# Kernel tuning notes

Hardware: AMD Instinct MI355X
Metric: run time of the kernel (lower is better)

The kernel has to match this reference:

```python
import jax, jax.numpy as jnp
import numpy as np

EPS = 1e-08


def _norm(H, add):
    # Faithful to GTN.norm: transpose, mask/set diagonal, row-normalize by degree, transpose back.
    # The original O(N^3) mm(deg_inv_diag, H) is expressed as an O(N^2) row scaling (same math).
    Ht = H.T
    n = Ht.shape[0]
    eye = jnp.eye(n, dtype=H.dtype)
    Ht = Ht * (1.0 - eye)
    if add:
        Ht = Ht + eye
    deg = jnp.sum(Ht, axis=1)
    deg_inv = jnp.where(deg == 0, 0.0, 1.0 / (deg + EPS))
    return (deg_inv[:, None] * Ht).T


def _gtconv(A, w):
    # A: [E, N, N]; w: [C, E, 1, 1] -> softmax over E, weighted sum of adjacency channels.
    s = jax.nn.softmax(w[:, :, 0, 0], axis=1)  # [C, E]
    return jnp.einsum('ce,eij->cij', s, A)     # [C, N, N]


def setup_inputs() -> dict:
    key = jax.random.key(0)
    k = jax.random.split(key, 6)
    E, N, C, w_in, w_out = 5, 2048, 2, 256, 64
    A = jax.random.uniform(k[0], (E, N, N), dtype=jnp.float32)
    X = jax.random.normal(k[1], (N, w_in), dtype=jnp.float32)
    conv_w_l0_1 = jax.random.normal(k[2], (C, E, 1, 1), dtype=jnp.float32)
    conv_w_l0_2 = jax.random.normal(k[3], (C, E, 1, 1), dtype=jnp.float32)
    conv_w_l1 = jax.random.normal(k[4], (C, E, 1, 1), dtype=jnp.float32)
    gcn_weight = jax.random.normal(k[5], (w_in, w_out), dtype=jnp.float32) * (1.0 / np.sqrt(w_in))
    return {"A": A, "X": X, "conv_w_l0_1": conv_w_l0_1, "conv_w_l0_2": conv_w_l0_2,
            "conv_w_l1": conv_w_l1, "gcn_weight": gcn_weight}


def reference(A, X, conv_w_l0_1, conv_w_l0_2, conv_w_l1, gcn_weight):
    N = A.shape[1]
    # Layer 0 (first=True): two GTConvs, meta-path composition via bmm.
    a = _gtconv(A, conv_w_l0_1)            # [C, N, N]
    b = _gtconv(A, conv_w_l0_2)            # [C, N, N]
    H = jnp.einsum('cij,cjk->cik', a, b)   # [C, N, N]
    # Layer 1 (first=False): normalize per channel, then compose with new conv.
    H = jax.vmap(lambda h: _norm(h, False))(H)
    a1 = _gtconv(A, conv_w_l1)
    H = jnp.einsum('cij,cjk->cik', H, a1)
    # GCN readout per channel: mm(norm_add(H_c).T, X @ W), relu, concat along features.
    Xw = X @ gcn_weight                     # [N, w_out]
    Hn = jax.vmap(lambda h: _norm(h, True))(H)   # [C, N, N]
    Xc = jax.nn.relu(jnp.einsum('cji,jk->cik', Hn, Xw))  # [C, N, w_out]
    X_ = jnp.transpose(Xc, (1, 0, 2)).reshape(N, -1)     # [N, C*w_out]
    return X_
```

## Files before the change

kernel.cpp:

```cpp
#include <hip/hip_runtime.h>
#include <cstdint>
#include <cstddef>

typedef unsigned short u16;
typedef __attribute__((ext_vector_type(8))) short short8;
typedef __attribute__((ext_vector_type(4))) float v4f;

static constexpr size_t NN = (size_t)2048 * 2048;
#define N2 2048

typedef __attribute__((address_space(1))) const unsigned int guint;
typedef __attribute__((address_space(3))) unsigned int luint;

__device__ __forceinline__ float b2f_bits(uint32_t hi) { union { uint32_t u; float f; } v; v.u = hi; return v.f; }
__device__ __forceinline__ float b2f(u16 x) { return b2f_bits((uint32_t)x << 16); }
__device__ __forceinline__ u16 f2b(float f) {
  union { float f; uint32_t u; } v; v.f = f;
  uint32_t r = v.u + 0x7fffu + ((v.u >> 16) & 1u);
  return (u16)(r >> 16);
}
__device__ __forceinline__ uint2 pack4(const float* f) {
  uint2 u;
  u.x = (uint32_t)f2b(f[0]) | ((uint32_t)f2b(f[1]) << 16);
  u.y = (uint32_t)f2b(f[2]) | ((uint32_t)f2b(f[3]) << 16);
  return u;
}
__device__ __forceinline__ uint4 pack8(const float* f) {
  uint4 u;
  u.x = (uint32_t)f2b(f[0]) | ((uint32_t)f2b(f[1]) << 16);
  u.y = (uint32_t)f2b(f[2]) | ((uint32_t)f2b(f[3]) << 16);
  u.z = (uint32_t)f2b(f[4]) | ((uint32_t)f2b(f[5]) << 16);
  u.w = (uint32_t)f2b(f[6]) | ((uint32_t)f2b(f[7]) << 16);
  return u;
}

__global__ __launch_bounds__(256, 6) void conv_kernel(
    const float* __restrict__ A, const float* __restrict__ w1,
    const float* __restrict__ w2, const float* __restrict__ w3,
    const float* __restrict__ X, const float* __restrict__ W,
    u16* __restrict__ abf, u16* __restrict__ bbt, u16* __restrict__ a1t,
    u16* __restrict__ Xwt)
{
  __shared__ float lb[32][33];
  __shared__ float la[32][33];
  const int t = threadIdx.x;
  const int i0 = blockIdx.y * 32, j0 = blockIdx.x * 32;

  float s1[2][5], s2[2][5], s3[2][5];
  {
    const float* wsrc[3] = { w1, w2, w3 };
    float (*sdst[3])[5] = { s1, s2, s3 };
    for (int q = 0; q < 3; ++q)
      for (int c = 0; c < 2; ++c) {
        float v[5], m = -1e30f, sum = 0.f;
        for (int e = 0; e < 5; ++e) { v[e] = wsrc[q][c * 5 + e]; m = fmaxf(m, v[e]); }
        for (int e = 0; e < 5; ++e) { v[e] = expf(v[e] - m); sum += v[e]; }
        for (int e = 0; e < 5; ++e) sdst[q][c][e] = v[e] / sum;
      }
  }

  const int row = t >> 3;
  const int c4 = (t & 7) * 4;
  float cst[2][4];

  {
    float fa[5][4];
    for (int e = 0; e < 5; ++e) {
      float4 v = *(const float4*)(A + (size_t)e * NN + (size_t)(i0 + row) * N2 + (j0 + c4));
      fa[e][0] = v.x; fa[e][1] = v.y; fa[e][2] = v.z; fa[e][3] = v.w;
    }
    for (int c = 0; c < 2; ++c) {
      float av[4] = {0,0,0,0}, bv[4] = {0,0,0,0}, cv[4] = {0,0,0,0};
      for (int e = 0; e < 5; ++e)
        #pragma unroll
        for (int u = 0; u < 4; ++u) {
          av[u] += s1[c][e] * fa[e][u];
          bv[u] += s2[c][e] * fa[e][u];
          cv[u] += s3[c][e] * fa[e][u];
        }
      *(uint2*)(abf + (size_t)c * NN + (size_t)(i0 + row) * N2 + (j0 + c4)) = pack4(av);
      float* ldst = (c == 0) ? &lb[row][c4] : &la[row][c4];
      #pragma unroll
      for (int u = 0; u < 4; ++u) ldst[u] = bv[u];
      #pragma unroll
      for (int u = 0; u < 4; ++u) cst[c][u] = cv[u];
    }
  }
  __syncthreads();
  {
    float t0[4], t1[4];
    #pragma unroll
    for (int u = 0; u < 4; ++u) { t0[u] = lb[c4 + u][row]; t1[u] = la[c4 + u][row]; }
    *(uint2*)(bbt + 0 * NN + (size_t)(j0 + row) * N2 + (i0 + c4)) = pack4(t0);
    *(uint2*)(bbt + 1 * NN + (size_t)(j0 + row) * N2 + (i0 + c4)) = pack4(t1);
  }
  __syncthreads();
  #pragma unroll
  for (int u = 0; u < 4; ++u) { lb[row][c4 + u] = cst[0][u]; la[row][c4 + u] = cst[1][u]; }
  __syncthreads();
  {
    float t0[4], t1[4];
    #pragma unroll
    for (int u = 0; u < 4; ++u) { t0[u] = lb[c4 + u][row]; t1[u] = la[c4 + u][row]; }
    *(uint2*)(a1t + 0 * NN + (size_t)(j0 + row) * N2 + (i0 + c4)) = pack4(t0);
    *(uint2*)(a1t + 1 * NN + (size_t)(j0 + row) * N2 + (i0 + c4)) = pack4(t1);
  }
  if (blockIdx.y < 8) {
    const int n = (int)(blockIdx.y * 64 + blockIdx.x) * 4 + (t >> 6);
    const int k = t & 63;
    float acc = 0.f;
    for (int m = 0; m < 256; ++m)
      acc += X[n * 256 + m] * W[m * 64 + k];
    Xwt[(size_t)k * N2 + n] = f2b(acc);
  }
}

template<bool TOUT>
__global__ __launch_bounds__(256, 5) void gemm_kernel(
    const u16* __restrict__ Ain, const u16* __restrict__ Btin,
    u16* __restrict__ Cout, float* __restrict__ csp, float* __restrict__ diag)
{
  const int c = blockIdx.z;
  const u16* Ac = Ain + (size_t)c * NN;
  const u16* Bc = Btin + (size_t)c * NN;
  const int m0 = blockIdx.y * 128, n0 = blockIdx.x * 64;
  const int t = threadIdx.x, w = t >> 6, lane = t & 63;
  const int quad = lane >> 4, r = lane & 15;
  __shared__ u16 SM[128 * 64 + 64 * 64];
  u16* As = SM;
  u16* Bs = SM + 128 * 64;

  v4f zero4 = { 0.f, 0.f, 0.f, 0.f };
  v4f acc[2][4];
  #pragma unroll
  for (int i = 0; i < 2; ++i)
    #pragma unroll
    for (int j = 0; j < 4; ++j) acc[i][j] = zero4;

  const int srow = lane >> 3;
  const int sgran = (lane & 7) ^ srow;

  for (int kt = 0; kt < 2048; kt += 64) {
    __syncthreads();
    #pragma unroll
    for (int i = 0; i < 4; ++i) {
      const int chunk = i * 4 + w;
      const u16* ga = Ac + (size_t)(m0 + chunk * 8 + srow) * N2 + kt + sgran * 8;
      __builtin_amdgcn_global_load_lds((guint*)ga, (luint*)(As + chunk * 512), 16, 0, 0);
    }
    #pragma unroll
    for (int i = 0; i < 2; ++i) {
      const int chunk = i * 4 + w;
      const u16* gb = Bc + (size_t)(n0 + chunk * 8 + srow) * N2 + kt + sgran * 8;
      __builtin_amdgcn_global_load_lds((guint*)gb, (luint*)(Bs + chunk * 512), 16, 0, 0);
    }
    __syncthreads();
    #pragma unroll
    for (int ks = 0; ks < 2; ++ks) {
      const int sl = ((ks * 4 + quad) ^ (r & 7)) * 8;
      short8 af[2], bf[4];
      #pragma unroll
      for (int i = 0; i < 2; ++i)
        af[i] = *(const short8*)(As + (w * 32 + i * 16 + r) * 64 + sl);
      #pragma unroll
      for (int j = 0; j < 4; ++j)
        bf[j] = *(const short8*)(Bs + (j * 16 + r) * 64 + sl);
      #pragma unroll
      for (int i = 0; i < 2; ++i)
        #pragma unroll
        for (int j = 0; j < 4; ++j)
          acc[i][j] = __builtin_amdgcn_mfma_f32_16x16x32_bf16(af[i], bf[j], acc[i][j], 0, 0, 0);
    }
  }
  if ((int)(blockIdx.x >> 1) == (int)blockIdx.y) {
    #pragma unroll
    for (int i = 0; i < 2; ++i) {
      const int rowg = m0 + w * 32 + i * 16 + quad * 4;
      #pragma unroll
      for (int j = 0; j < 4; ++j) {
        const int colg = n0 + j * 16 + r;
        #pragma unroll
        for (int g = 0; g < 4; ++g)
          if (rowg + g == colg) diag[c * N2 + colg] = acc[i][j][g];
      }
    }
  }
  if constexpr (!TOUT) {
    u16* Cc = Cout + (size_t)c * NN;
    #pragma unroll
    for (int i = 0; i < 2; ++i) {
      const int rowg = m0 + w * 32 + i * 16 + quad * 4;
      #pragma unroll
      for (int j = 0; j < 4; ++j) {
        const int colg = n0 + j * 16 + r;
        #pragma unroll
        for (int g = 0; g < 4; ++g)
          Cc[(size_t)(rowg + g) * N2 + colg] = f2b(acc[i][j][g]);
      }
    }
  }
  float s[4];
  #pragma unroll
  for (int j = 0; j < 4; ++j) {
    s[j] = 0.f;
    #pragma unroll
    for (int i = 0; i < 2; ++i)
      #pragma unroll
      for (int g = 0; g < 4; ++g) s[j] += acc[i][j][g];
    s[j] += __shfl_xor(s[j], 16);
    s[j] += __shfl_xor(s[j], 32);
  }
  __syncthreads();
  float* csl = (float*)SM;
  if (quad == 0) {
    #pragma unroll
    for (int j = 0; j < 4; ++j) csl[w * 64 + j * 16 + r] = s[j];
  }
  __syncthreads();
  if (t < 64) {
    const float v = csl[t] + csl[64 + t] + csl[128 + t] + csl[192 + t];
    csp[((size_t)(c * 16) + blockIdx.y) * N2 + n0 + t] = v;
  }
  if constexpr (TOUT) {
    __syncthreads();
    u16* tb = SM;
    #pragma unroll
    for (int i = 0; i < 2; ++i) {
      #pragma unroll
      for (int j = 0; j < 4; ++j) {
        #pragma unroll
        for (int g = 0; g < 4; ++g)
          tb[(j * 16 + r) * 136 + (w * 32 + i * 16 + quad * 4 + g)] = f2b(acc[i][j][g]);
      }
    }
    __syncthreads();
    u16* Cc = Cout + (size_t)c * NN;
    const int rown = t >> 2, seg = t & 3;
    const u16* ps = tb + rown * 136 + seg * 32;
    uint4* pd = (uint4*)(Cc + (size_t)(n0 + rown) * N2 + m0 + seg * 32);
    pd[0] = ((const uint4*)ps)[0];
    pd[1] = ((const uint4*)ps)[1];
    pd[2] = ((const uint4*)ps)[2];
    pd[3] = ((const uint4*)ps)[3];
  }
}

__global__ void colinv_kernel(const float* __restrict__ csp, const float* __restrict__ diag, float* __restrict__ ci)
{
  const int idx = blockIdx.x * 256 + threadIdx.x;
  float cs = 0.f;
  const int c = idx >> 11, q = idx & 2047;
  #pragma unroll
  for (int s = 0; s < 16; ++s) cs += csp[((size_t)(c * 16) + s) * N2 + q];
  const float deg = cs - diag[idx];
  ci[idx] = (deg == 0.f) ? 0.f : 1.f / (deg + 1e-8f);
}

__global__ __launch_bounds__(256) void scale_kernel(const u16* __restrict__ H, const float* __restrict__ ci, u16* __restrict__ Hn)
{
  const int idx = blockIdx.x * 256 + threadIdx.x;
  const int q0 = (idx & 255) * 8;
  const int p = (idx >> 8) & 2047;
  const int c = idx >> 19;
  const u16* src = H + (size_t)c * NN + (size_t)p * N2 + q0;
  const float* cv = ci + c * N2 + q0;
  uint4 hu = *(const uint4*)src;
  float h[8];
  h[0] = b2f_bits(hu.x << 16); h[1] = b2f_bits(hu.x & 0xffff0000u);
  h[2] = b2f_bits(hu.y << 16); h[3] = b2f_bits(hu.y & 0xffff0000u);
  h[4] = b2f_bits(hu.z << 16); h[5] = b2f_bits(hu.z & 0xffff0000u);
  h[6] = b2f_bits(hu.w << 16); h[7] = b2f_bits(hu.w & 0xffff0000u);
  float f[8];
  #pragma unroll
  for (int u = 0; u < 8; ++u) {
    float v = h[u] * cv[u];
    f[u] = (q0 + u == p) ? 0.f : v;
  }
  *(uint4*)(Hn + (size_t)c * NN + (size_t)p * N2 + q0) = pack8(f);
}

__global__ __launch_bounds__(256) void tgemm_kernel(
    const u16* __restrict__ H2t, const u16* __restrict__ Xwt, float* __restrict__ Tp)
{
  const int c = blockIdx.z, split = blockIdx.y;
  const int m0 = blockIdx.x * 128;
  const u16* Ac = H2t + (size_t)c * NN;
  const int t = threadIdx.x, w = t >> 6, lane = t & 63;
  const int quad = lane >> 4, r = lane & 15;
  __shared__ u16 As[128 * 64];
  __shared__ u16 Bs[64 * 64];

  v4f zero4 = { 0.f, 0.f, 0.f, 0.f };
  v4f acc[2][4];
  #pragma unroll
  for (int i = 0; i < 2; ++i)
    #pragma unroll
    for (int j = 0; j < 4; ++j) acc[i][j] = zero4;

  const int srow = lane >> 3;
  const int sgran = (lane & 7) ^ srow;

  for (int kk = 0; kk < 2; ++kk) {
    const int kt = split * 128 + kk * 64;
    __syncthreads();
    #pragma unroll
    for (int i = 0; i < 4; ++i) {
      const int chunk = i * 4 + w;
      const u16* ga = Ac + (size_t)(m0 + chunk * 8 + srow) * N2 + kt + sgran * 8;
      __builtin_amdgcn_global_load_lds((guint*)ga, (luint*)(As + chunk * 512), 16, 0, 0);
    }
    #pragma unroll
    for (int i = 0; i < 2; ++i) {
      const int chunk = i * 4 + w;
      const u16* gb = Xwt + (size_t)(chunk * 8 + srow) * N2 + kt + sgran * 8;
      __builtin_amdgcn_global_load_lds((guint*)gb, (luint*)(Bs + chunk * 512), 16, 0, 0);
    }
    __syncthreads();
    #pragma unroll
    for (int ks = 0; ks < 2; ++ks) {
      const int sl = ((ks * 4 + quad) ^ (r & 7)) * 8;
      short8 af[2], bf[4];
      #pragma unroll
      for (int i = 0; i < 2; ++i)
        af[i] = *(const short8*)(As + (w * 32 + i * 16 + r) * 64 + sl);
      #pragma unroll
      for (int j = 0; j < 4; ++j)
        bf[j] = *(const short8*)(Bs + (j * 16 + r) * 64 + sl);
      #pragma unroll
      for (int i = 0; i < 2; ++i)
        #pragma unroll
        for (int j = 0; j < 4; ++j)
          acc[i][j] = __builtin_amdgcn_mfma_f32_16x16x32_bf16(af[i], bf[j], acc[i][j], 0, 0, 0);
    }
  }
  const size_t pbase = (size_t)(split * 2 + c) * 2048;
  #pragma unroll
  for (int i = 0; i < 2; ++i) {
    const int rowg = m0 + w * 32 + i * 16 + quad * 4;
    #pragma unroll
    for (int j = 0; j < 4; ++j) {
      const int colg = j * 16 + r;
      #pragma unroll
      for (int g = 0; g < 4; ++g)
        Tp[(pbase + rowg + g) * 64 + colg] = acc[i][j][g];
    }
  }
}

__global__ void epilogue_kernel(const float* __restrict__ Tp, const float* __restrict__ cspb,
                                const float* __restrict__ diag2, const u16* __restrict__ Xwt,
                                float* __restrict__ out)
{
  const int idx = blockIdx.x * 256 + threadIdx.x;
  const int k = idx & 63;
  const int c = (idx >> 6) & 1;
  const int i = idx >> 7;
  float T = 0.f, cs = 0.f;
  #pragma unroll
  for (int s = 0; s < 16; ++s) {
    T  += Tp[((size_t)(s * 2 + c) * 2048 + i) * 64 + k];
    cs += cspb[((size_t)(c * 16) + s) * N2 + i];
  }
  const float hd = diag2[c * N2 + i];
  const float xw = b2f(Xwt[(size_t)k * N2 + i]);
  const float deg = cs - hd + 1.0f;
  const float dinv = (deg == 0.f) ? 0.f : 1.f / (deg + 1e-8f);
  float v = dinv * (T - hd * xw + xw);
  v = v > 0.f ? v : 0.f;
  out[(size_t)i * 128 + c * 64 + k] = v;
}

extern "C" void kernel_launch(void* const* d_in, const int* in_sizes, int n_in,
                              void* d_out, int out_size, void* d_ws, size_t ws_size,
                              hipStream_t stream) {
  const float* A  = (const float*)d_in[0];
  const float* X  = (const float*)d_in[1];
  const float* w1 = (const float*)d_in[2];
  const float* w2 = (const float*)d_in[3];
  const float* w3 = (const float*)d_in[4];
  const float* W  = (const float*)d_in[5];
  float* out = (float*)d_out;
  char* ws = (char*)d_ws;

  u16*   abf   = (u16*)(ws + 0);
  u16*   bbt   = (u16*)(ws + 16777216);
  u16*   a1t   = (u16*)(ws + 33554432);
  u16*   Hbf   = (u16*)(ws + 50331648);
  u16*   Hn    = (u16*)(ws + 67108864);
  u16*   Xwt   = (u16*)(ws + 83886080);
  float* cspa  = (float*)(ws + 84148224);
  float* cspb  = (float*)(ws + 84410368);
  float* diag1 = (float*)(ws + 84672512);
  float* diag2 = (float*)(ws + 84688896);
  float* ci1   = (float*)(ws + 84705280);
  u16*   H2t   = (u16*)(ws + 0);
  float* Tp    = (float*)(ws + 16777216);

  conv_kernel<<<dim3(64, 64), 256, 0, stream>>>(A, w1, w2, w3, X, W, abf, bbt, a1t, Xwt);
  gemm_kernel<false><<<dim3(32, 16, 2), 256, 0, stream>>>(abf, bbt, Hbf, cspa, diag1);
  colinv_kernel<<<16, 256, 0, stream>>>(cspa, diag1, ci1);
  scale_kernel<<<4096, 256, 0, stream>>>(Hbf, ci1, Hn);
  gemm_kernel<true><<<dim3(32, 16, 2), 256, 0, stream>>>(Hn, a1t, H2t, cspb, diag2);
  tgemm_kernel<<<dim3(16, 16, 2), 256, 0, stream>>>(H2t, Xwt, Tp);
  epilogue_kernel<<<1024, 256, 0, stream>>>(Tp, cspb, diag2, Xwt, out);
}
```

Measured before the change: 266.5 us.

## Split-K the two large GEMMs into two partial outputs merged downstream

Each big N×N GEMM now runs as a split-K over two halves of K, doubling the grid from 1024 to 2048 blocks for better CU occupancy. Each half writes its own bf16 partial product, column-sum partials and diagonal. Consumers (colinv, scale, tgemm, epilogue) sum the two partials, and launch bounds rise to 6 waves per SIMD. The cost is extra memory traffic for writing and re-reading the doubled partial matrices, plus a bf16 rounding of each partial before the add. The workspace layout is reshuffled with several dead pointer assignments.

Result: slower. 353.7 us (+32.7%).

```diff
diff --git a/kernel.cpp b/kernel.cpp
--- a/kernel.cpp
+++ b/kernel.cpp
@@ -32,6 +32,19 @@
   u.z = (uint32_t)f2b(f[4]) | ((uint32_t)f2b(f[5]) << 16);
   u.w = (uint32_t)f2b(f[6]) | ((uint32_t)f2b(f[7]) << 16);
   return u;
+}
+__device__ __forceinline__ void unpack8u(uint4 u, float* f) {
+  f[0] = b2f_bits(u.x << 16); f[1] = b2f_bits(u.x & 0xffff0000u);
+  f[2] = b2f_bits(u.y << 16); f[3] = b2f_bits(u.y & 0xffff0000u);
+  f[4] = b2f_bits(u.z << 16); f[5] = b2f_bits(u.z & 0xffff0000u);
+  f[6] = b2f_bits(u.w << 16); f[7] = b2f_bits(u.w & 0xffff0000u);
+}
+__device__ __forceinline__ uint4 add_bf16x8(uint4 a, uint4 b) {
+  float fa[8], fb[8], s[8];
+  unpack8u(a, fa); unpack8u(b, fb);
+  #pragma unroll
+  for (int u = 0; u < 8; ++u) s[u] = fa[u] + fb[u];
+  return pack8(s);
 }
 
 __global__ __launch_bounds__(256, 6) void conv_kernel(
@@ -116,11 +129,11 @@
 }
 
 template<bool TOUT>
-__global__ __launch_bounds__(256, 5) void gemm_kernel(
+__global__ __launch_bounds__(256, 6) void gemm_kernel(
     const u16* __restrict__ Ain, const u16* __restrict__ Btin,
-    u16* __restrict__ Cout, float* __restrict__ csp, float* __restrict__ diag)
-{
-  const int c = blockIdx.z;
+    u16* __restrict__ Cout, float* __restrict__ csp, float* __restrict__ diagp)
+{
+  const int c = (int)blockIdx.z >> 1, split = (int)blockIdx.z & 1;
   const u16* Ac = Ain + (size_t)c * NN;
   const u16* Bc = Btin + (size_t)c * NN;
   const int m0 = blockIdx.y * 128, n0 = blockIdx.x * 64;
@@ -140,7 +153,8 @@
   const int srow = lane >> 3;
   const int sgran = (lane & 7) ^ srow;
 
-  for (int kt = 0; kt < 2048; kt += 64) {
+  const int koff = split << 10;
+  for (int kt = koff; kt < koff + 1024; kt += 64) {
     __syncthreads();
     #pragma unroll
     for (int i = 0; i < 4; ++i) {
@@ -172,6 +186,7 @@
           acc[i][j] = __builtin_amdgcn_mfma_f32_16x16x32_bf16(af[i], bf[j], acc[i][j], 0, 0, 0);
     }
   }
+  u16* Cc = Cout + (size_t)(split * 2 + c) * NN;
   if ((int)(blockIdx.x >> 1) == (int)blockIdx.y) {
     #pragma unroll
     for (int i = 0; i < 2; ++i) {
@@ -181,12 +196,11 @@
         const int colg = n0 + j * 16 + r;
         #pragma unroll
         for (int g = 0; g < 4; ++g)
-          if (rowg + g == colg) diag[c * N2 + colg] = acc[i][j][g];
+          if (rowg + g == colg) diagp[(split * 2 + c) * N2 + colg] = acc[i][j][g];
       }
     }
   }
   if constexpr (!TOUT) {
-    u16* Cc = Cout + (size_t)c * NN;
     #pragma unroll
     for (int i = 0; i < 2; ++i) {
       const int rowg = m0 + w * 32 + i * 16 + quad * 4;
@@ -219,7 +233,7 @@
   __syncthreads();
   if (t < 64) {
     const float v = csl[t] + csl[64 + t] + csl[128 + t] + csl[192 + t];
-    csp[((size_t)(c * 16) + blockIdx.y) * N2 + n0 + t] = v;
+    csp[((size_t)(c * 32) + split * 16 + blockIdx.y) * N2 + n0 + t] = v;
   }
   if constexpr (TOUT) {
     __syncthreads();
@@ -234,7 +248,6 @@
       }
     }
     __syncthreads();
-    u16* Cc = Cout + (size_t)c * NN;
     const int rown = t >> 2, seg = t & 3;
     const u16* ps = tb + rown * 136 + seg * 32;
     uint4* pd = (uint4*)(Cc + (size_t)(n0 + rown) * N2 + m0 + seg * 32);
@@ -245,46 +258,44 @@
   }
 }
 
-__global__ void colinv_kernel(const float* __restrict__ csp, const float* __restrict__ diag, float* __restrict__ ci)
+__global__ void colinv_kernel(const float* __restrict__ csp, const float* __restrict__ diagp, float* __restrict__ ci)
 {
   const int idx = blockIdx.x * 256 + threadIdx.x;
   float cs = 0.f;
   const int c = idx >> 11, q = idx & 2047;
   #pragma unroll
-  for (int s = 0; s < 16; ++s) cs += csp[((size_t)(c * 16) + s) * N2 + q];
-  const float deg = cs - diag[idx];
+  for (int s = 0; s < 32; ++s) cs += csp[((size_t)(c * 32) + s) * N2 + q];
+  const float deg = cs - diagp[c * N2 + q] - diagp[(2 + c) * N2 + q];
   ci[idx] = (deg == 0.f) ? 0.f : 1.f / (deg + 1e-8f);
 }
 
-__global__ __launch_bounds__(256) void scale_kernel(const u16* __restrict__ H, const float* __restrict__ ci, u16* __restrict__ Hn)
+__global__ __launch_bounds__(256) void scale_kernel(const u16* __restrict__ H1p, const float* __restrict__ ci, u16* __restrict__ Hn)
 {
   const int idx = blockIdx.x * 256 + threadIdx.x;
   const int q0 = (idx & 255) * 8;
   const int p = (idx >> 8) & 2047;
   const int c = idx >> 19;
-  const u16* src = H + (size_t)c * NN + (size_t)p * N2 + q0;
+  const size_t off = (size_t)p * N2 + q0;
+  uint4 u0 = *(const uint4*)(H1p + (size_t)c * NN + off);
+  uint4 u1 = *(const uint4*)(H1p + (size_t)(2 + c) * NN + off);
   const float* cv = ci + c * N2 + q0;
-  uint4 hu = *(const uint4*)src;
-  float h[8];
-  h[0] = b2f_bits(hu.x << 16); h[1] = b2f_bits(hu.x & 0xffff0000u);
-  h[2] = b2f_bits(hu.y << 16); h[3] = b2f_bits(hu.y & 0xffff0000u);
-  h[4] = b2f_bits(hu.z << 16); h[5] = b2f_bits(hu.z & 0xffff0000u);
-  h[6] = b2f_bits(hu.w << 16); h[7] = b2f_bits(hu.w & 0xffff0000u);
-  float f[8];
+  float h0[8], h1[8], f[8];
+  unpack8u(u0, h0); unpack8u(u1, h1);
   #pragma unroll
   for (int u = 0; u < 8; ++u) {
-    float v = h[u] * cv[u];
+    float v = (h0[u] + h1[u]) * cv[u];
     f[u] = (q0 + u == p) ? 0.f : v;
   }
-  *(uint4*)(Hn + (size_t)c * NN + (size_t)p * N2 + q0) = pack8(f);
+  *(uint4*)(Hn + (size_t)c * NN + off) = pack8(f);
 }
 
 __global__ __launch_bounds__(256) void tgemm_kernel(
-    const u16* __restrict__ H2t, const u16* __restrict__ Xwt, float* __restrict__ Tp)
-{
-  const int c = blockIdx.z, split = blockIdx.y;
+    const u16* __restrict__ H2tp, const u16* __restrict__ Xwt, float* __restrict__ Tp)
+{
+  const int c = blockIdx.z, jsplit = blockIdx.y;
   const int m0 = blockIdx.x * 128;
-  const u16* Ac = H2t + (size_t)c * NN;
+  const u16* P0 = H2tp + (size_t)c * NN;
+  const u16* P1 = H2tp + (size_t)(2 + c) * NN;
   const int t = threadIdx.x, w = t >> 6, lane = t & 63;
   const int quad = lane >> 4, r = lane & 15;
   __shared__ u16 As[128 * 64];
@@ -301,20 +312,21 @@
   const int sgran = (lane & 7) ^ srow;
 
   for (int kk = 0; kk < 2; ++kk) {
-    const int kt = split * 128 + kk * 64;
-    __syncthreads();
-    #pragma unroll
-    for (int i = 0; i < 4; ++i) {
-      const int chunk = i * 4 + w;
-      const u16* ga = Ac + (size_t)(m0 + chunk * 8 + srow) * N2 + kt + sgran * 8;
-      __builtin_amdgcn_global_load_lds((guint*)ga, (luint*)(As + chunk * 512), 16, 0, 0);
-    }
+    const int kt = jsplit * 128 + kk * 64;
+    __syncthreads();
     #pragma unroll
     for (int i = 0; i < 2; ++i) {
       const int chunk = i * 4 + w;
       const u16* gb = Xwt + (size_t)(chunk * 8 + srow) * N2 + kt + sgran * 8;
       __builtin_amdgcn_global_load_lds((guint*)gb, (luint*)(Bs + chunk * 512), 16, 0, 0);
     }
+    #pragma unroll
+    for (int i = 0; i < 4; ++i) {
+      const int chunk = i * 4 + w;
+      const size_t off = (size_t)(m0 + chunk * 8 + srow) * N2 + kt + sgran * 8;
+      uint4 va = add_bf16x8(*(const uint4*)(P0 + off), *(const uint4*)(P1 + off));
+      *(uint4*)(As + chunk * 512 + lane * 8) = va;
+    }
     __syncthreads();
     #pragma unroll
     for (int ks = 0; ks < 2; ++ks) {
@@ -333,7 +345,7 @@
           acc[i][j] = __builtin_amdgcn_mfma_f32_16x16x32_bf16(af[i], bf[j], acc[i][j], 0, 0, 0);
     }
   }
-  const size_t pbase = (size_t)(split * 2 + c) * 2048;
+  const size_t pbase = (size_t)(jsplit * 2 + c) * 2048;
   #pragma unroll
   for (int i = 0; i < 2; ++i) {
     const int rowg = m0 + w * 32 + i * 16 + quad * 4;
@@ -348,7 +360,7 @@
 }
 
 __global__ void epilogue_kernel(const float* __restrict__ Tp, const float* __restrict__ cspb,
-                                const float* __restrict__ diag2, const u16* __restrict__ Xwt,
+                                const float* __restrict__ diag2p, const u16* __restrict__ Xwt,
                                 float* __restrict__ out)
 {
   const int idx = blockIdx.x * 256 + threadIdx.x;
@@ -357,11 +369,12 @@
   const int i = idx >> 7;
   float T = 0.f, cs = 0.f;
   #pragma unroll
-  for (int s = 0; s < 16; ++s) {
-    T  += Tp[((size_t)(s * 2 + c) * 2048 + i) * 64 + k];
-    cs += cspb[((size_t)(c * 16) + s) * N2 + i];
-  }
-  const float hd = diag2[c * N2 + i];
+  for (int s = 0; s < 16; ++s)
+    T += Tp[((size_t)(s * 2 + c) * 2048 + i) * 64 + k];
+  #pragma unroll
+  for (int s = 0; s < 32; ++s)
+    cs += cspb[((size_t)(c * 32) + s) * N2 + i];
+  const float hd = diag2p[c * N2 + i] + diag2p[(2 + c) * N2 + i];
   const float xw = b2f(Xwt[(size_t)k * N2 + i]);
   const float deg = cs - hd + 1.0f;
   const float dinv = (deg == 0.f) ? 0.f : 1.f / (deg + 1e-8f);
@@ -382,25 +395,28 @@
   float* out = (float*)d_out;
   char* ws = (char*)d_ws;
 
-  u16*   abf   = (u16*)(ws + 0);
-  u16*   bbt   = (u16*)(ws + 16777216);
-  u16*   a1t   = (u16*)(ws + 33554432);
-  u16*   Hbf   = (u16*)(ws + 50331648);
-  u16*   Hn    = (u16*)(ws + 67108864);
-  u16*   Xwt   = (u16*)(ws + 83886080);
-  float* cspa  = (float*)(ws + 84148224);
-  float* cspb  = (float*)(ws + 84410368);
-  float* diag1 = (float*)(ws + 84672512);
-  float* diag2 = (float*)(ws + 84688896);
-  float* ci1   = (float*)(ws + 84705280);
-  u16*   H2t   = (u16*)(ws + 0);
-  float* Tp    = (float*)(ws + 16777216);
+  u16*   abf    = (u16*)(ws + 0);
+  u16*   bbt    = (u16*)(ws + 16777216);
+  u16*   a1t    = (u16*)(ws + 33554432);
+  u16*   H1p    = (u16*)(ws + 50331648);
+  u16*   Hn     = (u16*)(ws + 16777216);
+  u16*   H2tp   = (u16*)(ws + 0);
+  float* Tp     = (float*)(ws + 83886080 + 262144 + 1048576 + 65536 + 16384);
+  u16*   Xwt    = (u16*)(ws + 83886080);
+  float* cspa   = (float*)(ws + 84148224);
+  float* cspb   = (float*)(ws + 84672512);
+  float* diag1p = (float*)(ws + 85196800);
+  float* diag2p = (float*)(ws + 85229568);
+  float* ci1    = (float*)(ws + 85262336);
+  u16*   H2tpB  = (u16*)(ws + 50331648);
+  Tp            = (float*)(ws + 85278720);
+  Tp            = (float*)(ws + 0);
 
   conv_kernel<<<dim3(64, 64), 256, 0, stream>>>(A, w1, w2, w3, X, W, abf, bbt, a1t, Xwt);
-  gemm_kernel<false><<<dim3(32, 16, 2), 256, 0, stream>>>(abf, bbt, Hbf, cspa, diag1);
-  colinv_kernel<<<16, 256, 0, stream>>>(cspa, diag1, ci1);
-  scale_kernel<<<4096, 256, 0, stream>>>(Hbf, ci1, Hn);
-  gemm_kernel<true><<<dim3(32, 16, 2), 256, 0, stream>>>(Hn, a1t, H2t, cspb, diag2);
-  tgemm_kernel<<<dim3(16, 16, 2), 256, 0, stream>>>(H2t, Xwt, Tp);
-  epilogue_kernel<<<1024, 256, 0, stream>>>(Tp, cspb, diag2, Xwt, out);
-}
+  gemm_kernel<false><<<dim3(32, 16, 4), 256, 0, stream>>>(abf, bbt, H1p, cspa, diag1p);
+  colinv_kernel<<<16, 256, 0, stream>>>(cspa, diag1p, ci1);
+  scale_kernel<<<4096, 256, 0, stream>>>(H1p, ci1, Hn);
+  gemm_kernel<true><<<dim3(32, 16, 4), 256, 0, stream>>>(Hn, a1t, H2tpB, cspb, diag2p);
+  tgemm_kernel<<<dim3(16, 16, 2), 256, 0, stream>>>(H2tpB, Xwt, Tp);
+  epilogue_kernel<<<1024, 256, 0, stream>>>(Tp, cspb, diag2p, Xwt, out);
+}
```
